# Optimization experiments

Hardware: AMD Instinct MI355X
Metric: run time of the kernel (lower is better)

The kernel has to match this reference:

```python
import jax, jax.numpy as jnp
import numpy as np

N, P, D, FDIM, TFEAT = 65536, 6, 256, 8, 16
RAW_DIM = 4 + TFEAT  # 20
IN_DIM = 3 + FDIM + 3 + 3  # xyz + frame embedding + rigid xyz + viewdir = 17


def setup_inputs() -> dict:
    key = jax.random.key(0)
    ks = jax.random.split(key, 16)
    inp = {
        "tpts": jax.random.normal(ks[0], (N, P, 3), jnp.float32),
        "bigpts": jax.random.normal(ks[1], (N, P, 3), jnp.float32),
        "viewdir": jax.random.normal(ks[2], (N, P, 3), jnp.float32),
        "dists": jax.random.uniform(ks[3], (N,), jnp.float32),
        "part_dist": jax.random.uniform(ks[4], (1, N, P), jnp.float32),
        "frame_dim": jax.random.normal(ks[5], (FDIM,), jnp.float32),
        "W1": jax.random.normal(ks[6], (P, IN_DIM, D), jnp.float32) / np.sqrt(IN_DIM),
        "b1": jax.random.normal(ks[7], (P, D), jnp.float32) * 0.01,
        "W2": jax.random.normal(ks[8], (P, D, D), jnp.float32) / np.sqrt(D),
        "b2": jax.random.normal(ks[9], (P, D), jnp.float32) * 0.01,
        "W3": jax.random.normal(ks[10], (P, D, RAW_DIM), jnp.float32) / np.sqrt(D),
        "b3": jax.random.normal(ks[11], (P, RAW_DIM), jnp.float32) * 0.01,
        "Wocc": jax.random.normal(ks[12], (P, D, 1), jnp.float32) / np.sqrt(D),
        "bocc": jax.random.normal(ks[13], (P, 1), jnp.float32) * 0.01,
        "tflag": jax.random.randint(ks[14], (N, P), 0, 2).astype(bool),
    }
    return inp


def _part_mlps(tpts, bigpts, viewdir, frame_dim, W1, b1, W2, b2, W3, b3, Wocc, bocc):
    # Run all P part networks on all N points (batched per-part GEMMs).
    n = tpts.shape[0]
    frame = jnp.broadcast_to(frame_dim, (n, P, FDIM))
    x = jnp.concatenate([tpts, frame, bigpts, viewdir], axis=-1)  # (N,P,17)
    h = jax.nn.relu(jnp.einsum('npi,pid->npd', x, W1) + b1)
    h = jax.nn.relu(jnp.einsum('npd,pde->npe', h, W2) + b2)
    raw_p = jnp.einsum('npd,pdr->npr', h, W3) + b3               # (N,P,20)
    occ_p = jax.nn.sigmoid(jnp.einsum('npd,pdo->npo', h, Wocc) + bocc)  # (N,P,1)
    return raw_p, occ_p


def reference(tpts, bigpts, viewdir, dists, part_dist, frame_dim,
              W1, b1, W2, b2, W3, b3, Wocc, bocc, tflag):
    raw_p, occ_p = _part_mlps(tpts, bigpts, viewdir, frame_dim,
                              W1, b1, W2, b2, W3, b3, Wocc, bocc)
    # scatter-back equivalent: unflagged (point, part) slots stay zero
    flag = tflag[..., None].astype(raw_p.dtype)  # (N,P,1)
    raws = raw_p * flag                           # (N,P,20)
    occs = occ_p * flag                           # (N,P,1)
    # cfg.aggr == 'mean'
    raw = raws.mean(axis=1)                       # (N,20)
    occ = occs.mean(axis=1)                       # (N,1)
    tocc = occs[..., 0]                           # (N,P)
    return jnp.concatenate([raw, occ, tocc], axis=-1)  # (N, 20+1+P)
```

## Files before the change

kernel.cpp:

```cpp
#include <hip/hip_runtime.h>
#include <hip/hip_bf16.h>

using bf16 = __hip_bfloat16;
typedef __bf16 bf16x8 __attribute__((ext_vector_type(8)));
typedef __bf16 bf16x4v __attribute__((ext_vector_type(4)));
typedef float f32x4 __attribute__((ext_vector_type(4)));

#define MFMA16(a, b, c) __builtin_amdgcn_mfma_f32_16x16x32_bf16((a), (b), (c), 0, 0, 0)


__global__ void prep_kernel(const float* __restrict__ W1, const float* __restrict__ b1,
                            const float* __restrict__ W2, const float* __restrict__ W3,
                            const float* __restrict__ Wocc, __bf16* __restrict__ ws) {
  const int b = blockIdx.x;
  const int tid = threadIdx.x;
  if (b < 96) {
    __shared__ float tile[64][65];
    const int p = b >> 4, t = b & 15;
    const int d0 = (t >> 2) * 64, e0 = (t & 3) * 64;
    const int lane = tid & 63, grp = tid >> 6;
    const float* src = W2 + p * 65536 + (d0 + grp * 16) * 256 + e0 + lane;
#pragma unroll
    for (int i = 0; i < 16; ++i) tile[grp * 16 + i][lane] = src[i * 256];
    __syncthreads();
#pragma unroll
    for (int q = 0; q < 2; ++q) {
      const int m = tid + q * 256;
      const int ee = m >> 3, c = m & 7;
      bf16x8 v;
#pragma unroll
      for (int j = 0; j < 8; ++j) v[j] = (__bf16)tile[c * 8 + j][ee];
      *reinterpret_cast<bf16x8*>(
          &ws[49152 + p * 65536 + (e0 + ee) * 256 + d0 + c * 8]) = v;
    }
    return;
  }
  const int t = 49152 + (b - 96) * 256 + tid;
  if (t < 55296) {
    const int u = t - 49152;
    const int p = u >> 10, r = u & 1023, n = r >> 2, c = r & 3;
    bf16x8 v;
#pragma unroll
    for (int j = 0; j < 8; ++j) {
      const int k = c * 8 + j;
      float x = 0.f;
      if (k < 17) {
        const int ko = (k < 8) ? k + 3 : ((k < 11) ? k - 8 : k);
        x = W1[p * 4352 + ko * 256 + n];
      } else if (k == 17) {
        x = b1[p * 256 + n];
      }
      v[j] = (__bf16)x;
    }
    *reinterpret_cast<bf16x8*>(&ws[p * 8192 + n * 32 + c * 8]) = v;
  } else if (t < 61440) {
    const int u = t - 55296;
    const int p = u >> 10, r = u & 1023, row = r >> 5, c = r & 31;
    bf16x8 v;
#pragma unroll
    for (int j = 0; j < 8; ++j) {
      const int k = c * 8 + j;
      float x = 0.f;
      if (row < 20)       x = W3[p * 5120 + k * 20 + row];
      else if (row == 20) x = Wocc[p * 256 + k];
      v[j] = (__bf16)x;
    }
    *reinterpret_cast<bf16x8*>(&ws[442368 + p * 8192 + row * 256 + c * 8]) = v;
  }
}

__global__ __launch_bounds__(256, 2) void tpose_main(
    const float* __restrict__ tpts, const float* __restrict__ bigpts,
    const float* __restrict__ viewdir, const float* __restrict__ frame,
    const float* __restrict__ b2g, const float* __restrict__ b3g,
    const float* __restrict__ boccg, const int* __restrict__ tflag,
    const __bf16* __restrict__ ws, float* __restrict__ out) {
  const __bf16* __restrict__ W1t = ws;
  const __bf16* __restrict__ W2t = ws + 49152;
  const __bf16* __restrict__ W3t = ws + 442368;

  __shared__ __align__(16) __bf16 Xf[128 * 40];
  __shared__ __align__(16) __bf16 Hf[128 * 256];
  __shared__ float Tocc[128 * 6];

  const int tid = threadIdx.x;
  const int w = tid >> 6;
  const int lane = tid & 63;
  const int lq = lane >> 4;
  const int ln = lane & 15;
  const int e = ln & 7;
  const int n0 = blockIdx.x * 128;

  if (tid < 128) {
    bf16x8 f8;
#pragma unroll
    for (int j = 0; j < 8; ++j) f8[j] = (__bf16)frame[j];
    *reinterpret_cast<bf16x8*>(&Xf[tid * 40]) = f8;
    bf16x8 z = {};
    z[1] = (__bf16)1.0f;
    *reinterpret_cast<bf16x8*>(&Xf[tid * 40 + 16]) = z;
    bf16x8 z2 = {};
    *reinterpret_cast<bf16x8*>(&Xf[tid * 40 + 24]) = z2;
  }

  const int role = tid & 3;
  const float* __restrict__ dynsrc =
      (role == 0) ? tpts : (role == 1) ? bigpts : viewdir;

  float pre[2][3];
  float flv[2];
#pragma unroll
  for (int pass = 0; pass < 2; ++pass) {
    const int pt = (tid >> 2) + pass * 64;
    const int base3 = (n0 + pt) * 18;
#pragma unroll
    for (int i = 0; i < 3; ++i) pre[pass][i] = dynsrc[base3 + i];
  }
#pragma unroll
  for (int s = 0; s < 2; ++s)
    flv[s] = (tflag[(n0 + w * 32 + s * 16 + ln) * 6] != 0) ? 1.f : 0.f;

  float psum0[2][4] = {{0.f, 0.f, 0.f, 0.f}, {0.f, 0.f, 0.f, 0.f}};
  float psum1[2][4] = {{0.f, 0.f, 0.f, 0.f}, {0.f, 0.f, 0.f, 0.f}};

  for (int p = 0; p < 6; ++p) {
    if (role < 3) {
#pragma unroll
      for (int pass = 0; pass < 2; ++pass) {
        const int pt = (tid >> 2) + pass * 64;
#pragma unroll
        for (int i = 0; i < 3; ++i)
          Xf[pt * 40 + 8 + role * 3 + i] = (__bf16)pre[pass][i];
      }
    }

    bf16x8 aw[4];
#pragma unroll
    for (int mt = 0; mt < 4; ++mt)
      aw[mt] = *reinterpret_cast<const bf16x8*>(
          &W1t[p * 8192 + (w * 64 + mt * 16 + ln) * 32 + lq * 8]);

    __syncthreads();

    f32x4 acc[4][8];
#pragma unroll
    for (int mt = 0; mt < 4; ++mt)
#pragma unroll
      for (int nt = 0; nt < 8; ++nt) acc[mt][nt] = f32x4{0.f, 0.f, 0.f, 0.f};
#pragma unroll
    for (int nt = 0; nt < 8; ++nt) {
      const bf16x8 xb =
          *reinterpret_cast<const bf16x8*>(&Xf[(nt * 16 + ln) * 40 + lq * 8]);
#pragma unroll
      for (int mt = 0; mt < 4; ++mt) acc[mt][nt] = MFMA16(aw[mt], xb, acc[mt][nt]);
    }
#pragma unroll
    for (int mt = 0; mt < 4; ++mt) {
      const int c = w * 8 + mt * 2 + (lq >> 1);
      const int off = ((c ^ e) << 3) + (lq & 1) * 4;
#pragma unroll
      for (int nt = 0; nt < 8; ++nt) {
        bf16x4v hv;
#pragma unroll
        for (int r = 0; r < 4; ++r) hv[r] = (__bf16)fmaxf(acc[mt][nt][r], 0.f);
        *reinterpret_cast<bf16x4v*>(&Hf[(nt * 16 + ln) * 256 + off]) = hv;
      }
    }

    __syncthreads();

    const __bf16* __restrict__ w2p = W2t + p * 65536 + (w * 64 + ln) * 256 + lq * 8;
    bf16x8 a2[4];
#pragma unroll
    for (int mt = 0; mt < 4; ++mt)
      a2[mt] = *reinterpret_cast<const bf16x8*>(w2p + mt * 4096);
    f32x4 b2v[4];
#pragma unroll
    for (int mt = 0; mt < 4; ++mt)
      b2v[mt] = *reinterpret_cast<const f32x4*>(
          &b2g[p * 256 + w * 64 + mt * 16 + lq * 4]);

    const int pn = (p < 5) ? p + 1 : 5;
    float fln[2];
#pragma unroll
    for (int pass = 0; pass < 2; ++pass) {
      const int pt = (tid >> 2) + pass * 64;
      const int base3 = ((n0 + pt) * 6 + pn) * 3;
#pragma unroll
      for (int i = 0; i < 3; ++i) pre[pass][i] = dynsrc[base3 + i];
    }
#pragma unroll
    for (int s = 0; s < 2; ++s)
      fln[s] = (tflag[(n0 + w * 32 + s * 16 + ln) * 6 + pn] != 0) ? 1.f : 0.f;

#pragma unroll
    for (int mt = 0; mt < 4; ++mt)
#pragma unroll
      for (int nt = 0; nt < 8; ++nt) acc[mt][nt] = b2v[mt];
    {
#pragma unroll
      for (int kk = 0; kk < 8; ++kk) {
        bf16x8 a2n[4];
        if (kk < 7) {
#pragma unroll
          for (int mt = 0; mt < 4; ++mt)
            a2n[mt] = *reinterpret_cast<const bf16x8*>(
                w2p + mt * 4096 + (kk + 1) * 32);
        }
#pragma unroll
        for (int nt = 0; nt < 8; ++nt) {
          const bf16x8 hb = *reinterpret_cast<const bf16x8*>(
              &Hf[(nt * 16 + ln) * 256 + (((kk * 4 + lq) ^ e) << 3)]);
#pragma unroll
          for (int mt = 0; mt < 4; ++mt) acc[mt][nt] = MFMA16(a2[mt], hb, acc[mt][nt]);
        }
#pragma unroll
        for (int mt = 0; mt < 4; ++mt) a2[mt] = a2n[mt];
      }
    }

    __syncthreads();

#pragma unroll
    for (int mt = 0; mt < 4; ++mt) {
      const int c = w * 8 + mt * 2 + (lq >> 1);
      const int off = ((c ^ e) << 3) + (lq & 1) * 4;
#pragma unroll
      for (int nt = 0; nt < 8; ++nt) {
        bf16x4v hv;
#pragma unroll
        for (int r = 0; r < 4; ++r) hv[r] = (__bf16)fmaxf(acc[mt][nt][r], 0.f);
        *reinterpret_cast<bf16x4v*>(&Hf[(nt * 16 + ln) * 256 + off]) = hv;
      }
    }

    __syncthreads();

    f32x4 acc3[2][2];
    {
      float b3v[2][4];
#pragma unroll
      for (int mt = 0; mt < 2; ++mt)
#pragma unroll
        for (int r = 0; r < 4; ++r) {
          const int d = mt * 16 + lq * 4 + r;
          float v = 0.f;
          if (d < 20)       v = b3g[p * 20 + d];
          else if (d == 20) v = boccg[p];
          b3v[mt][r] = v;
        }
#pragma unroll
      for (int mt = 0; mt < 2; ++mt)
#pragma unroll
        for (int s = 0; s < 2; ++s)
#pragma unroll
          for (int r = 0; r < 4; ++r) acc3[mt][s][r] = b3v[mt][r];
    }
    const __bf16* __restrict__ w3p = W3t + p * 8192 + ln * 256 + lq * 8;
#pragma unroll
    for (int kk = 0; kk < 8; ++kk) {
      bf16x8 a3[2];
#pragma unroll
      for (int mt = 0; mt < 2; ++mt)
        a3[mt] = *reinterpret_cast<const bf16x8*>(w3p + mt * 4096 + kk * 32);
#pragma unroll
      for (int s = 0; s < 2; ++s) {
        const bf16x8 hb = *reinterpret_cast<const bf16x8*>(
            &Hf[(w * 32 + s * 16 + ln) * 256 + (((kk * 4 + lq) ^ e) << 3)]);
#pragma unroll
        for (int mt = 0; mt < 2; ++mt) acc3[mt][s] = MFMA16(a3[mt], hb, acc3[mt][s]);
      }
    }

#pragma unroll
    for (int s = 0; s < 2; ++s) {
#pragma unroll
      for (int r = 0; r < 4; ++r) psum0[s][r] += flv[s] * acc3[0][s][r];
      if (lq == 0) {
#pragma unroll
        for (int r = 0; r < 4; ++r) psum1[s][r] += flv[s] * acc3[1][s][r];
      } else if (lq == 1) {
        const float occ = 1.f / (1.f + __expf(-acc3[1][s][0]));
        Tocc[(w * 32 + s * 16 + ln) * 6 + p] = flv[s] * occ;
        psum1[s][0] += flv[s] * occ;
      }
    }

    flv[0] = fln[0];
    flv[1] = fln[1];
  }

  __syncthreads();
  float* stage = reinterpret_cast<float*>(Hf);
  const float inv6 = 1.f / 6.f;
#pragma unroll
  for (int s = 0; s < 2; ++s) {
    const int ptl = w * 32 + s * 16 + ln;
#pragma unroll
    for (int r = 0; r < 4; ++r) stage[ptl * 27 + lq * 4 + r] = psum0[s][r] * inv6;
    if (lq == 0) {
#pragma unroll
      for (int r = 0; r < 4; ++r) stage[ptl * 27 + 16 + r] = psum1[s][r] * inv6;
    } else if (lq == 1) {
      stage[ptl * 27 + 20] = psum1[s][0] * inv6;
    }
  }
  if (tid < 128) {
#pragma unroll
    for (int pp = 0; pp < 6; ++pp) stage[tid * 27 + 21 + pp] = Tocc[tid * 6 + pp];
  }
  __syncthreads();
  float* outp = out + (size_t)n0 * 27;
#pragma unroll
  for (int q = 0; q < 4; ++q) {
    const int m = tid + q * 256;
    if (m < 864)
      *reinterpret_cast<f32x4*>(&outp[m * 4]) =
          *reinterpret_cast<const f32x4*>(&stage[m * 4]);
  }
}

extern "C" void kernel_launch(void* const* d_in, const int* in_sizes, int n_in,
                              void* d_out, int out_size, void* d_ws, size_t ws_size,
                              hipStream_t stream) {
  const float* tpts    = (const float*)d_in[0];
  const float* bigpts  = (const float*)d_in[1];
  const float* viewdir = (const float*)d_in[2];
  const float* frame   = (const float*)d_in[5];
  const float* W1      = (const float*)d_in[6];
  const float* b1      = (const float*)d_in[7];
  const float* W2      = (const float*)d_in[8];
  const float* b2      = (const float*)d_in[9];
  const float* W3      = (const float*)d_in[10];
  const float* b3      = (const float*)d_in[11];
  const float* Wocc    = (const float*)d_in[12];
  const float* bocc    = (const float*)d_in[13];
  const int*   tflag   = (const int*)d_in[14];
  __bf16* ws  = (__bf16*)d_ws;
  float*  out = (float*)d_out;

  prep_kernel<<<144, 256, 0, stream>>>(W1, b1, W2, W3, Wocc, ws);
  tpose_main<<<512, 256, 0, stream>>>(tpts, bigpts, viewdir, frame, b2, b3,
                                      bocc, tflag, ws, out);
}
```

Measured before the change: 192.4 us.

## Split per-block work across 8 waves instead of 4 in main kernel

```diff
diff --git a/kernel.cpp b/kernel.cpp
--- a/kernel.cpp
+++ b/kernel.cpp
@@ -69,7 +69,7 @@
   }
 }
 
-__global__ __launch_bounds__(256, 2) void tpose_main(
+__global__ __launch_bounds__(512, 4) void tpose_main(
     const float* __restrict__ tpts, const float* __restrict__ bigpts,
     const float* __restrict__ viewdir, const float* __restrict__ frame,
     const float* __restrict__ b2g, const float* __restrict__ b3g,
@@ -106,45 +106,38 @@
   const int role = tid & 3;
   const float* __restrict__ dynsrc =
       (role == 0) ? tpts : (role == 1) ? bigpts : viewdir;
-
-  float pre[2][3];
-  float flv[2];
-#pragma unroll
-  for (int pass = 0; pass < 2; ++pass) {
-    const int pt = (tid >> 2) + pass * 64;
-    const int base3 = (n0 + pt) * 18;
-#pragma unroll
-    for (int i = 0; i < 3; ++i) pre[pass][i] = dynsrc[base3 + i];
-  }
-#pragma unroll
-  for (int s = 0; s < 2; ++s)
-    flv[s] = (tflag[(n0 + w * 32 + s * 16 + ln) * 6] != 0) ? 1.f : 0.f;
-
-  float psum0[2][4] = {{0.f, 0.f, 0.f, 0.f}, {0.f, 0.f, 0.f, 0.f}};
-  float psum1[2][4] = {{0.f, 0.f, 0.f, 0.f}, {0.f, 0.f, 0.f, 0.f}};
+  const int ppt = tid >> 2;
+
+  float pre[3];
+  float flv;
+  {
+    const int base3 = (n0 + ppt) * 18;
+#pragma unroll
+    for (int i = 0; i < 3; ++i) pre[i] = dynsrc[base3 + i];
+  }
+  flv = (tflag[(n0 + w * 16 + ln) * 6] != 0) ? 1.f : 0.f;
+
+  float psum0[4] = {0.f, 0.f, 0.f, 0.f};
+  float psum1[4] = {0.f, 0.f, 0.f, 0.f};
 
   for (int p = 0; p < 6; ++p) {
     if (role < 3) {
 #pragma unroll
-      for (int pass = 0; pass < 2; ++pass) {
-        const int pt = (tid >> 2) + pass * 64;
-#pragma unroll
-        for (int i = 0; i < 3; ++i)
-          Xf[pt * 40 + 8 + role * 3 + i] = (__bf16)pre[pass][i];
-      }
-    }
-
-    bf16x8 aw[4];
-#pragma unroll
-    for (int mt = 0; mt < 4; ++mt)
+      for (int i = 0; i < 3; ++i)
+        Xf[ppt * 40 + 8 + role * 3 + i] = (__bf16)pre[i];
+    }
+
+    bf16x8 aw[2];
+#pragma unroll
+    for (int mt = 0; mt < 2; ++mt)
       aw[mt] = *reinterpret_cast<const bf16x8*>(
-          &W1t[p * 8192 + (w * 64 + mt * 16 + ln) * 32 + lq * 8]);
-
-    __syncthreads();
-
-    f32x4 acc[4][8];
-#pragma unroll
-    for (int mt = 0; mt < 4; ++mt)
+          &W1t[p * 8192 + (w * 32 + mt * 16 + ln) * 32 + lq * 8]);
+
+    __syncthreads();
+
+    f32x4 acc[2][8];
+#pragma unroll
+    for (int mt = 0; mt < 2; ++mt)
 #pragma unroll
       for (int nt = 0; nt < 8; ++nt) acc[mt][nt] = f32x4{0.f, 0.f, 0.f, 0.f};
 #pragma unroll
@@ -152,11 +145,11 @@
       const bf16x8 xb =
           *reinterpret_cast<const bf16x8*>(&Xf[(nt * 16 + ln) * 40 + lq * 8]);
 #pragma unroll
-      for (int mt = 0; mt < 4; ++mt) acc[mt][nt] = MFMA16(aw[mt], xb, acc[mt][nt]);
-    }
-#pragma unroll
-    for (int mt = 0; mt < 4; ++mt) {
-      const int c = w * 8 + mt * 2 + (lq >> 1);
+      for (int mt = 0; mt < 2; ++mt) acc[mt][nt] = MFMA16(aw[mt], xb, acc[mt][nt]);
+    }
+#pragma unroll
+    for (int mt = 0; mt < 2; ++mt) {
+      const int c = w * 4 + mt * 2 + (lq >> 1);
       const int off = ((c ^ e) << 3) + (lq & 1) * 4;
 #pragma unroll
       for (int nt = 0; nt < 8; ++nt) {
@@ -169,41 +162,37 @@
 
     __syncthreads();
 
-    const __bf16* __restrict__ w2p = W2t + p * 65536 + (w * 64 + ln) * 256 + lq * 8;
-    bf16x8 a2[4];
-#pragma unroll
-    for (int mt = 0; mt < 4; ++mt)
+    const __bf16* __restrict__ w2p = W2t + p * 65536 + (w * 32 + ln) * 256 + lq * 8;
+    bf16x8 a2[2];
+#pragma unroll
+    for (int mt = 0; mt < 2; ++mt)
       a2[mt] = *reinterpret_cast<const bf16x8*>(w2p + mt * 4096);
-    f32x4 b2v[4];
-#pragma unroll
-    for (int mt = 0; mt < 4; ++mt)
+    f32x4 b2v[2];
+#pragma unroll
+    for (int mt = 0; mt < 2; ++mt)
       b2v[mt] = *reinterpret_cast<const f32x4*>(
-          &b2g[p * 256 + w * 64 + mt * 16 + lq * 4]);
+          &b2g[p * 256 + w * 32 + mt * 16 + lq * 4]);
 
     const int pn = (p < 5) ? p + 1 : 5;
-    float fln[2];
-#pragma unroll
-    for (int pass = 0; pass < 2; ++pass) {
-      const int pt = (tid >> 2) + pass * 64;
-      const int base3 = ((n0 + pt) * 6 + pn) * 3;
-#pragma unroll
-      for (int i = 0; i < 3; ++i) pre[pass][i] = dynsrc[base3 + i];
-    }
-#pragma unroll
-    for (int s = 0; s < 2; ++s)
-      fln[s] = (tflag[(n0 + w * 32 + s * 16 + ln) * 6 + pn] != 0) ? 1.f : 0.f;
-
-#pragma unroll
-    for (int mt = 0; mt < 4; ++mt)
+    float fln;
+    {
+      const int base3 = ((n0 + ppt) * 6 + pn) * 3;
+#pragma unroll
+      for (int i = 0; i < 3; ++i) pre[i] = dynsrc[base3 + i];
+    }
+    fln = (tflag[(n0 + w * 16 + ln) * 6 + pn] != 0) ? 1.f : 0.f;
+
+#pragma unroll
+    for (int mt = 0; mt < 2; ++mt)
 #pragma unroll
       for (int nt = 0; nt < 8; ++nt) acc[mt][nt] = b2v[mt];
     {
 #pragma unroll
       for (int kk = 0; kk < 8; ++kk) {
-        bf16x8 a2n[4];
+        bf16x8 a2n[2];
         if (kk < 7) {
 #pragma unroll
-          for (int mt = 0; mt < 4; ++mt)
+          for (int mt = 0; mt < 2; ++mt)
             a2n[mt] = *reinterpret_cast<const bf16x8*>(
                 w2p + mt * 4096 + (kk + 1) * 32);
         }
@@ -212,18 +201,18 @@
           const bf16x8 hb = *reinterpret_cast<const bf16x8*>(
               &Hf[(nt * 16 + ln) * 256 + (((kk * 4 + lq) ^ e) << 3)]);
 #pragma unroll
-          for (int mt = 0; mt < 4; ++mt) acc[mt][nt] = MFMA16(a2[mt], hb, acc[mt][nt]);
+          for (int mt = 0; mt < 2; ++mt) acc[mt][nt] = MFMA16(a2[mt], hb, acc[mt][nt]);
         }
 #pragma unroll
-        for (int mt = 0; mt < 4; ++mt) a2[mt] = a2n[mt];
+        for (int mt = 0; mt < 2; ++mt) a2[mt] = a2n[mt];
       }
     }
 
     __syncthreads();
 
 #pragma unroll
-    for (int mt = 0; mt < 4; ++mt) {
-      const int c = w * 8 + mt * 2 + (lq >> 1);
+    for (int mt = 0; mt < 2; ++mt) {
+      const int c = w * 4 + mt * 2 + (lq >> 1);
       const int off = ((c ^ e) << 3) + (lq & 1) * 4;
 #pragma unroll
       for (int nt = 0; nt < 8; ++nt) {
@@ -236,9 +225,8 @@
 
     __syncthreads();
 
-    f32x4 acc3[2][2];
+    f32x4 acc3[2];
     {
-      float b3v[2][4];
 #pragma unroll
       for (int mt = 0; mt < 2; ++mt)
 #pragma unroll
@@ -247,14 +235,8 @@
           float v = 0.f;
           if (d < 20)       v = b3g[p * 20 + d];
           else if (d == 20) v = boccg[p];
-          b3v[mt][r] = v;
+          acc3[mt][r] = v;
         }
-#pragma unroll
-      for (int mt = 0; mt < 2; ++mt)
-#pragma unroll
-        for (int s = 0; s < 2; ++s)
-#pragma unroll
-          for (int r = 0; r < 4; ++r) acc3[mt][s][r] = b3v[mt][r];
     }
     const __bf16* __restrict__ w3p = W3t + p * 8192 + ln * 256 + lq * 8;
 #pragma unroll
@@ -263,46 +245,38 @@
 #pragma unroll
       for (int mt = 0; mt < 2; ++mt)
         a3[mt] = *reinterpret_cast<const bf16x8*>(w3p + mt * 4096 + kk * 32);
-#pragma unroll
-      for (int s = 0; s < 2; ++s) {
-        const bf16x8 hb = *reinterpret_cast<const bf16x8*>(
-            &Hf[(w * 32 + s * 16 + ln) * 256 + (((kk * 4 + lq) ^ e) << 3)]);
-#pragma unroll
-        for (int mt = 0; mt < 2; ++mt) acc3[mt][s] = MFMA16(a3[mt], hb, acc3[mt][s]);
-      }
-    }
-
-#pragma unroll
-    for (int s = 0; s < 2; ++s) {
-#pragma unroll
-      for (int r = 0; r < 4; ++r) psum0[s][r] += flv[s] * acc3[0][s][r];
-      if (lq == 0) {
-#pragma unroll
-        for (int r = 0; r < 4; ++r) psum1[s][r] += flv[s] * acc3[1][s][r];
-      } else if (lq == 1) {
-        const float occ = 1.f / (1.f + __expf(-acc3[1][s][0]));
-        Tocc[(w * 32 + s * 16 + ln) * 6 + p] = flv[s] * occ;
-        psum1[s][0] += flv[s] * occ;
-      }
-    }
-
-    flv[0] = fln[0];
-    flv[1] = fln[1];
+      const bf16x8 hb = *reinterpret_cast<const bf16x8*>(
+          &Hf[(w * 16 + ln) * 256 + (((kk * 4 + lq) ^ e) << 3)]);
+#pragma unroll
+      for (int mt = 0; mt < 2; ++mt) acc3[mt] = MFMA16(a3[mt], hb, acc3[mt]);
+    }
+
+#pragma unroll
+    for (int r = 0; r < 4; ++r) psum0[r] += flv * acc3[0][r];
+    if (lq == 0) {
+#pragma unroll
+      for (int r = 0; r < 4; ++r) psum1[r] += flv * acc3[1][r];
+    } else if (lq == 1) {
+      const float occ = 1.f / (1.f + __expf(-acc3[1][0]));
+      Tocc[(w * 16 + ln) * 6 + p] = flv * occ;
+      psum1[0] += flv * occ;
+    }
+
+    flv = fln;
   }
 
   __syncthreads();
   float* stage = reinterpret_cast<float*>(Hf);
   const float inv6 = 1.f / 6.f;
-#pragma unroll
-  for (int s = 0; s < 2; ++s) {
-    const int ptl = w * 32 + s * 16 + ln;
-#pragma unroll
-    for (int r = 0; r < 4; ++r) stage[ptl * 27 + lq * 4 + r] = psum0[s][r] * inv6;
+  {
+    const int ptl = w * 16 + ln;
+#pragma unroll
+    for (int r = 0; r < 4; ++r) stage[ptl * 27 + lq * 4 + r] = psum0[r] * inv6;
     if (lq == 0) {
 #pragma unroll
-      for (int r = 0; r < 4; ++r) stage[ptl * 27 + 16 + r] = psum1[s][r] * inv6;
+      for (int r = 0; r < 4; ++r) stage[ptl * 27 + 16 + r] = psum1[r] * inv6;
     } else if (lq == 1) {
-      stage[ptl * 27 + 20] = psum1[s][0] * inv6;
+      stage[ptl * 27 + 20] = psum1[0] * inv6;
     }
   }
   if (tid < 128) {
@@ -312,8 +286,8 @@
   __syncthreads();
   float* outp = out + (size_t)n0 * 27;
 #pragma unroll
-  for (int q = 0; q < 4; ++q) {
-    const int m = tid + q * 256;
+  for (int q = 0; q < 2; ++q) {
+    const int m = tid + q * 512;
     if (m < 864)
       *reinterpret_cast<f32x4*>(&outp[m * 4]) =
           *reinterpret_cast<const f32x4*>(&stage[m * 4]);
@@ -340,6 +314,6 @@
   float*  out = (float*)d_out;
 
   prep_kernel<<<144, 256, 0, stream>>>(W1, b1, W2, W3, Wocc, ws);
-  tpose_main<<<512, 256, 0, stream>>>(tpts, bigpts, viewdir, frame, b2, b3,
+  tpose_main<<<512, 512, 0, stream>>>(tpts, bigpts, viewdir, frame, b2, b3,
                                       bocc, tflag, ws, out);
 }
```

Result: slower. 226.8 us (+17.9%).
